# Kernel tuning notes

Measured on AMD Instinct MI355X. Metric: run time of the kernel, lower is better.

Reference implementation:

```python
import jax, jax.numpy as jnp
import numpy as np
from jax import lax

B, C, H, W = 16, 256, 32, 32
HK, WK = 16, 16
NH = 8              # num_heads
HD = C // NH        # head_dim = 32
N = H * W           # 1024
M = HK * WK         # 256
EXP = 3             # attn_expansion
HID = NH * EXP      # 24 hidden channels in DLA
EPS = 1e-5


def setup_inputs() -> dict:
    key = jax.random.key(0)
    ks = jax.random.split(key, 16)
    s = 0.02
    return {
        "q": jax.random.normal(ks[0], (B, C, H, W), jnp.float32),
        "kv": jax.random.normal(ks[1], (B, C, HK, WK), jnp.float32),
        "Wq": jax.random.normal(ks[2], (C, C), jnp.float32) * s,
        "Wkv": jax.random.normal(ks[3], (2 * C, C), jnp.float32) * s,
        "Wp": jax.random.normal(ks[4], (C, C), jnp.float32) * s,
        "bp": jnp.zeros((C,), jnp.float32),
        "rpb": jnp.ones((N, M), jnp.float32),
        "W_exp": jax.random.normal(ks[5], (HID, NH), jnp.float32) * s,   # 1x1 conv heads->hidden
        "g1": jnp.ones((HID,), jnp.float32),
        "b1": jnp.zeros((HID,), jnp.float32),
        "W_dw": jax.random.normal(ks[6], (HID, 1, 3, 3), jnp.float32) * s,  # depthwise 3x3
        "g2": jnp.ones((HID,), jnp.float32),
        "b2": jnp.zeros((HID,), jnp.float32),
        "W_red": jax.random.normal(ks[7], (NH, HID), jnp.float32) * s,  # 1x1 conv hidden->heads
        "g3": jnp.ones((NH,), jnp.float32),
        "b3": jnp.zeros((NH,), jnp.float32),
    }


def group_norm(x, gamma, beta, groups):
    b, c, h, w = x.shape
    xg = x.reshape(b, groups, c // groups, h, w)
    mu = xg.mean(axis=(2, 3, 4), keepdims=True)
    var = xg.var(axis=(2, 3, 4), keepdims=True)
    xn = ((xg - mu) * lax.rsqrt(var + EPS)).reshape(b, c, h, w)
    return xn * gamma[None, :, None, None] + beta[None, :, None, None]


def swish(x):
    return x * jax.nn.sigmoid(x)


def dla(a, W_exp, g1, b1, W_dw, g2, b2, W_red, g3, b3):
    # a: [B, NH, N, M] treated as NCHW image with C=num_heads
    x = jnp.einsum('bcnm,oc->bonm', a, W_exp)              # 1x1 expand -> [B,HID,N,M]
    x = swish(group_norm(x, g1, b1, EXP))
    x = lax.conv_general_dilated(
        x, W_dw, window_strides=(1, 1), padding='SAME',
        feature_group_count=HID,
        dimension_numbers=('NCHW', 'OIHW', 'NCHW'))        # depthwise 3x3
    x = swish(group_norm(x, g2, b2, EXP))
    x = jnp.einsum('bcnm,oc->bonm', x, W_red)              # 1x1 reduce -> [B,NH,N,M]
    x = group_norm(x, g3, b3, 1)                            # no activation
    return x


def reference(q, kv, Wq, Wkv, Wp, bp, rpb, W_exp, g1, b1, W_dw, g2, b2, W_red, g3, b3):
    b = q.shape[0]
    scale = HD ** -0.5
    # kv path: [B,C,HK,WK] -> [B,M,C] -> Linear(C->2C)
    kv_t = kv.reshape(b, C, M).transpose(0, 2, 1)
    kvp = kv_t @ Wkv.T                                     # [B,M,2C]
    kvp = kvp.reshape(b, M, 2, NH, HD).transpose(2, 0, 3, 1, 4)  # [2,B,NH,M,HD]
    k, v = kvp[0], kvp[1]
    # q path: [B,C,H,W] -> [B,N,C] -> Linear -> [B,NH,N,HD]
    qf = (q.reshape(b, C, N).transpose(0, 2, 1) @ Wq.T)
    qh = qf.reshape(b, N, NH, HD).transpose(0, 2, 1, 3)
    attn = jnp.einsum('bhnd,bhmd->bhnm', qh, k) * scale + rpb[None, None]
    attn = jax.nn.softmax(attn, axis=-1)
    attn = dla(attn, W_exp, g1, b1, W_dw, g2, b2, W_red, g3, b3)
    out = jnp.einsum('bhnm,bhmd->bhnd', attn, v)           # [B,NH,N,HD]
    out = out.transpose(0, 2, 1, 3).reshape(b, N, C)
    out = out @ Wp.T + bp
    return out.transpose(0, 2, 1).reshape(b, C, H, W)
```

## Files before the change

### kernel.cpp

```cpp
#include <hip/hip_runtime.h>
#include <math.h>

#define Bb 16
#define Cc 256
#define Nn 1024
#define Mm 256
#define NHh 8
#define HDd 32
#define HIDh 24
#define NMs (Nn*Mm)
#define TTB 16
#define CHUNK 8
#define EPSf 1e-5f
#define SCALEf 0.17677669529663687f
#define STP 32

typedef float v2f __attribute__((ext_vector_type(2)));
typedef __attribute__((ext_vector_type(8))) short bf8v;
typedef __attribute__((ext_vector_type(4))) float f4v;

__device__ __forceinline__ float wave_sum(float v){
#pragma unroll
  for (int off=32; off; off>>=1) v += __shfl_xor(v, off, 64);
  return v;
}
__device__ __forceinline__ float sigm_(float x){ return __builtin_amdgcn_rcpf(1.f + __expf(-x)); }
__device__ __forceinline__ float swish_(float x){ return x * sigm_(x); }
__device__ __forceinline__ v2f swish2(v2f x){
  v2f r;
  r.x = x.x * sigm_(x.x);
  r.y = x.y * sigm_(x.y);
  return r;
}
__device__ __forceinline__ unsigned short f2bf(float f){
  unsigned u = __float_as_uint(f);
  u += 0x7fffu + ((u >> 16) & 1u);
  return (unsigned short)(u >> 16);
}
__device__ __forceinline__ unsigned cvtpk(float lo, float hi){
  unsigned r;
  asm("v_cvt_pk_bf16_f32 %0, %1, %2" : "=v"(r) : "v"(lo), "v"(hi));
  return r;
}
__device__ __forceinline__ float bfup(unsigned short s){ return __uint_as_float(((unsigned)s) << 16); }
__device__ __forceinline__ float bflo(unsigned u){ return __uint_as_float(u << 16); }
__device__ __forceinline__ float bfhi(unsigned u){ return __uint_as_float(u & 0xffff0000u); }
__device__ __forceinline__ void gload_lds16(const void* g, void* l){
  __builtin_amdgcn_global_load_lds(
      (const __attribute__((address_space(1))) unsigned int*)g,
      (__attribute__((address_space(3))) unsigned int*)l, 16, 0, 0);
}

template<int MODE>
__launch_bounds__(256)
__global__ void gemm_mfma(const float* __restrict__ A,
                          const float* __restrict__ W,
                          const float* __restrict__ bias,
                          float* __restrict__ O1, float* __restrict__ O2, int Isize)
{
  __shared__ __align__(16) unsigned short Wt[64 * 40];
  __shared__ __align__(16) unsigned short At[64 * 40];
  const int b = blockIdx.z;
  const int i0 = blockIdx.x * 64;
  const int j0 = blockIdx.y * 64;
  const int tid = threadIdx.x;
  const int lane = tid & 63, wv = tid >> 6;
  const int wj = (wv >> 1) * 32, wi = (wv & 1) * 32;
  const int l15 = lane & 15, l4 = lane >> 4;

  const float* Ab = A + (long)b * Cc * Isize;
  const int sj = tid >> 2, skh = (tid & 3) * 8;
  const int si = tid & 63, skb = (tid >> 6) * 8;

  f4v acc[2][2] = {};
  for (int k0 = 0; k0 < Cc; k0 += 32) {
    float wreg[8];
    {
      const float* wp = W + (long)(j0 + sj) * Cc + k0 + skh;
      *(f4v*)&wreg[0] = *(const f4v*)&wp[0];
      *(f4v*)&wreg[4] = *(const f4v*)&wp[4];
    }
    float areg[8];
    {
      const float* ap = Ab + (long)(k0 + skb) * Isize + i0 + si;
#pragma unroll
      for (int e = 0; e < 8; e++) areg[e] = ap[(long)e * Isize];
    }
    __syncthreads();
    {
      unsigned pk[4];
#pragma unroll
      for (int t = 0; t < 4; t++) pk[t] = cvtpk(wreg[2*t], wreg[2*t+1]);
      *(uint4*)&Wt[sj*40 + skh] = make_uint4(pk[0], pk[1], pk[2], pk[3]);
#pragma unroll
      for (int t = 0; t < 4; t++) pk[t] = cvtpk(areg[2*t], areg[2*t+1]);
      *(uint4*)&At[si*40 + skb] = make_uint4(pk[0], pk[1], pk[2], pk[3]);
    }
    __syncthreads();
    bf8v af[2], bf[2];
#pragma unroll
    for (int fm = 0; fm < 2; fm++)
      af[fm] = *(const bf8v*)&Wt[(wj + fm*16 + l15)*40 + l4*8];
#pragma unroll
    for (int fn = 0; fn < 2; fn++)
      bf[fn] = *(const bf8v*)&At[(wi + fn*16 + l15)*40 + l4*8];
#pragma unroll
    for (int fm = 0; fm < 2; fm++)
#pragma unroll
      for (int fn = 0; fn < 2; fn++)
        acc[fm][fn] = __builtin_amdgcn_mfma_f32_16x16x32_bf16(af[fm], bf[fn], acc[fm][fn], 0, 0, 0);
  }
#pragma unroll
  for (int fm = 0; fm < 2; fm++) {
    const int jb = j0 + wj + fm*16 + l4*4;
    f4v bv = {0.f, 0.f, 0.f, 0.f};
    if (MODE == 2) bv = *(const f4v*)&bias[jb];
#pragma unroll
    for (int fn = 0; fn < 2; fn++) {
      const int ii = i0 + wi + fn*16 + l15;
      if (MODE == 1) {
        const int two = jb >> 8, jj = jb & 255;
        const int h = jj >> 5, d0 = jj & 31;
        unsigned short* p = (unsigned short*)(two ? O2 : O1)
                          + (((long)b * NHh + h) * Mm + ii) * HDd + d0;
        *(uint2*)p = make_uint2(cvtpk(acc[fm][fn][0], acc[fm][fn][1]),
                                cvtpk(acc[fm][fn][2], acc[fm][fn][3]));
      } else {
        float* op = O1 + ((long)b * Cc + jb) * (long)Isize + ii;
#pragma unroll
        for (int r = 0; r < 4; r++)
          op[(long)r * Isize] = acc[fm][fn][r] + bv[r];
      }
    }
  }
}

__launch_bounds__(256)
__global__ void attn_softmax(const float* __restrict__ qhT, const unsigned short* __restrict__ kb,
                             const float* __restrict__ rpb, unsigned short* __restrict__ attn)
{
  __shared__ __align__(16) unsigned short Kt[Mm * 40];
  __shared__ __align__(16) unsigned short Qt[64 * 40];
  const int b = blockIdx.z, h = blockIdx.y, n0 = blockIdx.x * 64;
  const int tid = threadIdx.x;
  const int lane = tid & 63, wv = tid >> 6;
  const int l15 = lane & 15, l4 = lane >> 4;
  {
    const unsigned short* kp = kb + ((long)b * NHh + h) * Mm * HDd;
#pragma unroll
    for (int u = 0; u < 4; u++) {
      const int f = tid + u * 256;
      const int m = f >> 2, q8 = (f & 3) * 8;
      *(uint4*)&Kt[m * 40 + q8] = *(const uint4*)&kp[m * HDd + q8];
    }
  }
  {
    const float* qp = qhT + ((long)b * NHh + h) * HDd * Nn + n0;
#pragma unroll
    for (int u = 0; u < 4; u++) {
      const int f = tid + u * 256;
      const int n = f & 63, d2 = (f >> 6) * 2;
      const float q0 = qp[(long)d2 * Nn + n];
      const float q1 = qp[(long)(d2 + 1) * Nn + n];
      *(unsigned*)&Qt[n * 40 + d2] = cvtpk(q0, q1);
    }
  }
  __syncthreads();
  const bf8v qf = *(const bf8v*)&Qt[(wv * 16 + l15) * 40 + l4 * 8];
  f4v S[16];
#pragma unroll
  for (int mt = 0; mt < 16; mt++) {
    const bf8v kf = *(const bf8v*)&Kt[(mt * 16 + l15) * 40 + l4 * 8];
    f4v z = {0.f, 0.f, 0.f, 0.f};
    S[mt] = __builtin_amdgcn_mfma_f32_16x16x32_bf16(kf, qf, z, 0, 0, 0);
  }
  const int n = n0 + wv * 16 + l15;
  const float* rp = rpb + (long)n * Mm;
  float mx = -1e30f;
#pragma unroll
  for (int mt = 0; mt < 16; mt++) {
    const f4v r4 = *(const f4v*)&rp[mt * 16 + l4 * 4];
    S[mt][0] = fmaf(S[mt][0], SCALEf, r4.x);
    S[mt][1] = fmaf(S[mt][1], SCALEf, r4.y);
    S[mt][2] = fmaf(S[mt][2], SCALEf, r4.z);
    S[mt][3] = fmaf(S[mt][3], SCALEf, r4.w);
    mx = fmaxf(mx, fmaxf(fmaxf(S[mt][0], S[mt][1]), fmaxf(S[mt][2], S[mt][3])));
  }
  mx = fmaxf(mx, __shfl_xor(mx, 16, 64));
  mx = fmaxf(mx, __shfl_xor(mx, 32, 64));
  float sum = 0.f;
#pragma unroll
  for (int mt = 0; mt < 16; mt++) {
    S[mt][0] = __expf(S[mt][0] - mx);
    S[mt][1] = __expf(S[mt][1] - mx);
    S[mt][2] = __expf(S[mt][2] - mx);
    S[mt][3] = __expf(S[mt][3] - mx);
    sum += (S[mt][0] + S[mt][1]) + (S[mt][2] + S[mt][3]);
  }
  sum += __shfl_xor(sum, 16, 64);
  sum += __shfl_xor(sum, 32, 64);
  const float inv = __builtin_amdgcn_rcpf(sum);
  unsigned short* ap = attn + (((long)b * NHh + h) * Nn + n) * Mm;
#pragma unroll
  for (int mt = 0; mt < 16; mt++) {
    const unsigned p0 = cvtpk(S[mt][0] * inv, S[mt][1] * inv);
    const unsigned p1 = cvtpk(S[mt][2] * inv, S[mt][3] * inv);
    *(uint2*)&ap[mt * 16 + l4 * 4] = make_uint2(p0, p1);
  }
}

__launch_bounds__(256)
__global__ void gram_stats(const unsigned short* __restrict__ attn, float* __restrict__ G)
{
  __shared__ float red[36][4];
  const int b = blockIdx.y, tid = threadIdx.x;
  const unsigned short* ap = attn + (long)b * NHh * NMs + (long)blockIdx.x * 2048 + tid * 8;
  float a[8][8];
#pragma unroll
  for (int h = 0; h < 8; h++) {
    const uint4 v = *(const uint4*)&ap[(long)h * NMs];
    a[h][0] = bflo(v.x); a[h][1] = bfhi(v.x); a[h][2] = bflo(v.y); a[h][3] = bfhi(v.y);
    a[h][4] = bflo(v.z); a[h][5] = bfhi(v.z); a[h][6] = bflo(v.w); a[h][7] = bfhi(v.w);
  }
  float g[36];
  int t = 0;
#pragma unroll
  for (int i = 0; i < 8; i++)
#pragma unroll
    for (int j = i; j < 8; j++, t++) {
      float s = 0.f;
#pragma unroll
      for (int m = 0; m < 8; m++) s = fmaf(a[i][m], a[j][m], s);
      g[t] = s;
    }
  const int lane = tid & 63, wid = tid >> 6;
#pragma unroll
  for (int t2 = 0; t2 < 36; t2++) {
    const float s = wave_sum(g[t2]);
    if (lane == 0) red[t2][wid] = s;
  }
  __syncthreads();
  if (tid < 36)
    atomicAdd(&G[((long)b * 36 + tid) * STP],
              red[tid][0] + red[tid][1] + red[tid][2] + red[tid][3]);
}

__launch_bounds__(768, 6)
__global__ void dla_pass_b(const unsigned short* __restrict__ attn,
                           const float* __restrict__ Wexp,
                           const float* __restrict__ g1, const float* __restrict__ b1,
                           const float* __restrict__ G, const float* __restrict__ Wdw,
                           unsigned short* __restrict__ x2, float* __restrict__ stats2c, int b0)
{
  __shared__ __align__(16) unsigned short sl[(TTB + 2) * NHh * Mm];
  const int tid = threadIdx.x;
  const int wv = tid >> 6, lane = tid & 63;
  const int bc = blockIdx.y, b = b0 + bc;
  const int n0 = blockIdx.x * TTB;
  const int c0 = wv * 2;
  const int g = wv >> 2;

  {
    const unsigned short* abase = attn + (long)b * NHh * NMs;
    const int q_lo = lane >> 5;
    const int m0 = (lane & 31) * 8;
#pragma unroll
    for (int i = 0; i < 6; i++) {
      const int pp = (wv * 6 + i) * 2;
      const int row = pp >> 3;
      const int nn = n0 - 1 + row;
      if (nn >= 0 && nn < Nn) {
        const int h = (pp + q_lo) & 7;
        gload_lds16(abase + (long)h * NMs + (long)nn * Mm + m0, &sl[pp * Mm]);
      }
    }
  }

  float mu, rs;
  {
    const float* Gb = G + (long)b * 36 * STP;
    float sum = 0.f, sumsq = 0.f;
    for (int c = g * 8; c < g * 8 + 8; c++) {
      float w[8];
#pragma unroll
      for (int h = 0; h < 8; h++) w[h] = Wexp[c * 8 + h];
      float wsu = 0.f;
#pragma unroll
      for (int h = 0; h < 8; h++) wsu += w[h];
      sum += wsu;
      float s2 = 0.f;
      int t = 0;
#pragma unroll
      for (int i = 0; i < 8; i++)
#pragma unroll
        for (int j = i; j < 8; j++, t++) {
          const float f = (i == j) ? 1.f : 2.f;
          s2 = fmaf(f * w[i] * w[j], Gb[t * STP], s2);
        }
      sumsq += s2;
    }
    const float cnt = 8.f * NMs;
    mu = sum * ((float)Nn / cnt);
    const float var = sumsq / cnt - mu * mu;
    rs = rsqrtf(var + EPSf);
  }
  v2f we2[8], wd2[9], B12;
  {
    const float A10 = rs * g1[c0], A11 = rs * g1[c0 + 1];
    B12.x = b1[c0] - mu * A10;
    B12.y = b1[c0 + 1] - mu * A11;
#pragma unroll
    for (int h = 0; h < NHh; h++) {
      we2[h].x = Wexp[c0 * NHh + h] * A10;
      we2[h].y = Wexp[(c0 + 1) * NHh + h] * A11;
    }
#pragma unroll
    for (int k = 0; k < 9; k++) {
      wd2[k].x = Wdw[c0 * 9 + k];
      wd2[k].y = Wdw[(c0 + 1) * 9 + k];
    }
  }
  __syncthreads();

  v2f s1p[4] = {}, s2p[4] = {};
  v2f smp = {0.f, 0.f}, sqp = {0.f, 0.f};
  for (int r = -1; r <= TTB; r++) {
    const int nn = n0 + r;
    const bool rowv = (nn >= 0 && nn < Nn);
    v2f xp[4];
    if (rowv) {
#pragma unroll
      for (int mi = 0; mi < 4; mi++) xp[mi] = B12;
      const unsigned short* sp = &sl[(r + 1) * NHh * Mm + lane * 4];
#pragma unroll
      for (int h = 0; h < NHh; h++) {
        const ushort4 v = *(const ushort4*)&sp[h * Mm];
        xp[0] += we2[h] * bfup(v.x);
        xp[1] += we2[h] * bfup(v.y);
        xp[2] += we2[h] * bfup(v.z);
        xp[3] += we2[h] * bfup(v.w);
      }
#pragma unroll
      for (int mi = 0; mi < 4; mi++) xp[mi] = swish2(xp[mi]);
    } else {
#pragma unroll
      for (int mi = 0; mi < 4; mi++) xp[mi] = (v2f){0.f, 0.f};
    }
    v2f xl, xr;
    xl.x = __shfl_up(xp[3].x, 1);  xl.y = __shfl_up(xp[3].y, 1);
    xr.x = __shfl_down(xp[0].x, 1); xr.y = __shfl_down(xp[0].y, 1);
    if (lane == 0)  { xl = (v2f){0.f, 0.f}; }
    if (lane == 63) { xr = (v2f){0.f, 0.f}; }
    const v2f L[4] = {xl, xp[0], xp[1], xp[2]};
    const v2f R[4] = {xp[1], xp[2], xp[3], xr};
    v2f y[4];
#pragma unroll
    for (int mi = 0; mi < 4; mi++) {
      const v2f u0 = wd2[0] * L[mi] + wd2[1] * xp[mi] + wd2[2] * R[mi];
      const v2f u1 = wd2[3] * L[mi] + wd2[4] * xp[mi] + wd2[5] * R[mi];
      const v2f u2 = wd2[6] * L[mi] + wd2[7] * xp[mi] + wd2[8] * R[mi];
      y[mi] = s2p[mi] + u2;
      s2p[mi] = s1p[mi] + u1;
      s1p[mi] = u0;
    }
    if (r >= 1) {
#pragma unroll
      for (int mi = 0; mi < 4; mi++) {
        smp += y[mi];
        sqp += y[mi] * y[mi];
      }
      const int nw = n0 + r - 1;
      const unsigned w0 = cvtpk(y[0].x, y[1].x), w1 = cvtpk(y[2].x, y[3].x);
      const unsigned w2 = cvtpk(y[0].y, y[1].y), w3 = cvtpk(y[2].y, y[3].y);
      unsigned short* xq = x2 + ((long)(bc * Nn + nw) * HIDh + c0) * Mm + lane * 4;
      *(uint2*)xq        = make_uint2(w0, w1);
      *(uint2*)(xq + Mm) = make_uint2(w2, w3);
    }
  }
  {
    const float vs0 = wave_sum(smp.x), vq0 = wave_sum(sqp.x);
    const float vs1 = wave_sum(smp.y), vq1 = wave_sum(sqp.y);
    if (lane == 0) {
      atomicAdd(&stats2c[((long)b * HIDh + c0) * STP], vs0);
      atomicAdd(&stats2c[((long)b * HIDh + c0) * STP + 1], vq0);
      atomicAdd(&stats2c[((long)b * HIDh + c0 + 1) * STP], vs1);
      atomicAdd(&stats2c[((long)b * HIDh + c0 + 1) * STP + 1], vq1);
    }
  }
}

__launch_bounds__(256)
__global__ void dla_pass_c(const unsigned short* __restrict__ x2, const float* __restrict__ g2,
                           const float* __restrict__ b2, const float* __restrict__ stats2c,
                           const float* __restrict__ Wred, unsigned short* __restrict__ a2,
                           float* __restrict__ partial3, int b0)
{
  __shared__ float wA[HIDh], wB[HIDh], wrs[HIDh][NHh];
  __shared__ float red2s[2][4];
  const int tid = threadIdx.x;
  const int wv = tid >> 6, lane = tid & 63;
  const int bc = blockIdx.y, b = b0 + bc;
  if (tid < HIDh) {
    const int c = tid, g = c >> 3;
    float s = 0.f, q = 0.f;
#pragma unroll
    for (int cc = 0; cc < 8; cc++) {
      s += stats2c[((long)b * HIDh + g * 8 + cc) * STP];
      q += stats2c[((long)b * HIDh + g * 8 + cc) * STP + 1];
    }
    const float cnt = 8.f * NMs;
    const float mu = s / cnt;
    const float var = q / cnt - mu * mu;
    const float A2 = rsqrtf(var + EPSf) * g2[c];
    wA[c] = A2; wB[c] = b2[c] - mu * A2;
  }
  if (tid < HIDh * NHh) {
    const int c = tid >> 3, h = tid & 7;
    wrs[c][h] = Wred[h * HIDh + c];
  }
  __syncthreads();
  const int rsel = lane >> 5, ms = lane & 31;
  const int n = blockIdx.x * 8 + wv * 2 + rsel;
  const unsigned short* xp = x2 + (long)(bc * Nn + n) * HIDh * Mm + ms * 8;
  v2f red[NHh][4] = {};
#pragma unroll
  for (int c = 0; c < HIDh; c++) {
    const uint4 xv = *(const uint4*)&xp[c * Mm];
    const v2f A2 = {wA[c], wA[c]}, B2 = {wB[c], wB[c]};
    v2f xw[4];
    xw[0] = (v2f){bflo(xv.x), bfhi(xv.x)};
    xw[1] = (v2f){bflo(xv.y), bfhi(xv.y)};
    xw[2] = (v2f){bflo(xv.z), bfhi(xv.z)};
    xw[3] = (v2f){bflo(xv.w), bfhi(xv.w)};
#pragma unroll
    for (int mi = 0; mi < 4; mi++) xw[mi] = swish2(xw[mi] * A2 + B2);
#pragma unroll
    for (int h = 0; h < NHh; h++) {
      const float w = wrs[c][h];
      const v2f w2 = {w, w};
#pragma unroll
      for (int mi = 0; mi < 4; mi++) red[h][mi] += w2 * xw[mi];
    }
  }
  v2f s3v = {0.f, 0.f}, q3v = {0.f, 0.f};
#pragma unroll
  for (int h = 0; h < NHh; h++) {
    uint4 st;
    st.x = cvtpk(red[h][0].x, red[h][0].y);
    st.y = cvtpk(red[h][1].x, red[h][1].y);
    st.z = cvtpk(red[h][2].x, red[h][2].y);
    st.w = cvtpk(red[h][3].x, red[h][3].y);
    *(uint4*)&a2[(((long)b * NHh + h) * Nn + n) * Mm + ms * 8] = st;
#pragma unroll
    for (int mi = 0; mi < 4; mi++) {
      s3v += red[h][mi];
      q3v += red[h][mi] * red[h][mi];
    }
  }
  float s3 = s3v.x + s3v.y, q3 = q3v.x + q3v.y;
  s3 = wave_sum(s3); q3 = wave_sum(q3);
  if (lane == 0) { red2s[0][wv] = s3; red2s[1][wv] = q3; }
  __syncthreads();
  if (tid < 2) {
    float t = red2s[tid][0] + red2s[tid][1] + red2s[tid][2] + red2s[tid][3];
    partial3[((long)b * 128 + blockIdx.x) * 2 + tid] = t;
  }
}

__launch_bounds__(256)
__global__ void pv_mfma(const unsigned short* __restrict__ a2, const unsigned short* __restrict__ vb,
                        const float* __restrict__ partial3,
                        const float* __restrict__ g3, const float* __restrict__ b3,
                        float* __restrict__ o)
{
  __shared__ __align__(16) unsigned short Vt[32 * 264];
  __shared__ float svl[32][9];
  __shared__ float r4s[4];
  const int b = blockIdx.z, h = blockIdx.y, n0 = blockIdx.x * 128;
  const int tid = threadIdx.x;
  const int lane = tid & 63, wv = tid >> 6;
  const int l15 = lane & 15, l4 = lane >> 4;
  {
    const unsigned short* vp = vb + ((long)b * NHh + h) * Mm * HDd;
#pragma unroll
    for (int u = 0; u < 32; u++) {
      const int idx = tid + u * 256;
      const int m = idx >> 5, d = idx & 31;
      Vt[d * 264 + m] = vp[idx];
    }
  }
  float pv_;
  {
    const int half = tid >> 7, i = tid & 127;
    pv_ = partial3[((long)b * 128 + i) * 2 + half];
  }
  __syncthreads();
  {
    const int d = tid & 31, seg = tid >> 5;
    float s = 0.f;
#pragma unroll
    for (int mm = 0; mm < 32; mm++) s += bfup(Vt[d * 264 + seg * 32 + mm]);
    svl[d][seg] = s;
  }
  {
    const float w = wave_sum(pv_);
    if (lane == 0) r4s[wv] = w;
  }
  __syncthreads();
  if (tid < 32) {
    float t = 0.f;
#pragma unroll
    for (int seg = 0; seg < 8; seg++) t += svl[tid][seg];
    svl[tid][0] = t;
  }
  __syncthreads();
  const float cnt = (float)(NHh * NMs);
  const float mu = (r4s[0] + r4s[1]) / cnt;
  const float var = (r4s[2] + r4s[3]) / cnt - mu * mu;
  const float r3 = rsqrtf(var + EPSf);
  const float alpha = r3 * g3[h];
  const float beta = b3[h] - mu * alpha;

  const unsigned short* ap = a2 + (((long)b * NHh + h) * Nn + n0) * Mm;
  f4v acc[2][2] = {};
#pragma unroll 2
  for (int k0 = 0; k0 < Mm; k0 += 32) {
    bf8v af[2], bf[2];
#pragma unroll
    for (int fm = 0; fm < 2; fm++)
      af[fm] = *(const bf8v*)&Vt[(fm * 16 + l15) * 264 + k0 + l4 * 8];
#pragma unroll
    for (int fn = 0; fn < 2; fn++)
      bf[fn] = *(const bf8v*)&ap[(long)(wv * 32 + fn * 16 + l15) * Mm + k0 + l4 * 8];
#pragma unroll
    for (int fm = 0; fm < 2; fm++)
#pragma unroll
      for (int fn = 0; fn < 2; fn++)
        acc[fm][fn] = __builtin_amdgcn_mfma_f32_16x16x32_bf16(af[fm], bf[fn], acc[fm][fn], 0, 0, 0);
  }
#pragma unroll
  for (int fm = 0; fm < 2; fm++) {
#pragma unroll
    for (int r = 0; r < 4; r++) {
      const int d = fm * 16 + l4 * 4 + r;
      const float bv = beta * svl[d][0];
      float* op = o + ((long)b * Cc + h * HDd + d) * Nn + n0 + wv * 32 + l15;
#pragma unroll
      for (int fn = 0; fn < 2; fn++)
        op[fn * 16] = fmaf(alpha, acc[fm][fn][r], bv);
    }
  }
}

extern "C" void kernel_launch(void* const* d_in, const int* in_sizes, int n_in,
                              void* d_out, int out_size, void* d_ws, size_t ws_size,
                              hipStream_t stream) {
  const float* q    = (const float*)d_in[0];
  const float* kv   = (const float*)d_in[1];
  const float* Wq   = (const float*)d_in[2];
  const float* Wkv  = (const float*)d_in[3];
  const float* Wp   = (const float*)d_in[4];
  const float* bp   = (const float*)d_in[5];
  const float* rpb  = (const float*)d_in[6];
  const float* Wexp = (const float*)d_in[7];
  const float* g1   = (const float*)d_in[8];
  const float* b1   = (const float*)d_in[9];
  const float* Wdw  = (const float*)d_in[10];
  const float* g2   = (const float*)d_in[11];
  const float* b2   = (const float*)d_in[12];
  const float* Wred = (const float*)d_in[13];
  const float* g3   = (const float*)d_in[14];
  const float* b3   = (const float*)d_in[15];
  float* out = (float*)d_out;

  float* ws = (float*)d_ws;
  size_t off = 0;
  auto alloc = [&](size_t n) { float* p = ws + off; off += n; return p; };
  float* attnf   = alloc((size_t)Bb * NHh * NMs / 2);
  float* a2f     = alloc((size_t)Bb * NHh * NMs / 2);
  float* big     = alloc((size_t)CHUNK * HIDh * NMs / 2);
  float* kbuf    = alloc((size_t)Bb * NHh * Mm * HDd);
  float* vbuf    = alloc((size_t)Bb * NHh * Mm * HDd);
  float* G       = alloc((size_t)Bb * 36 * STP);
  float* stats2c = alloc((size_t)Bb * HIDh * STP);
  float* partial3= alloc((size_t)Bb * 128 * 2);
  unsigned short* attn = (unsigned short*)attnf;
  unsigned short* a2 = (unsigned short*)a2f;
  unsigned short* kb16 = (unsigned short*)kbuf;
  unsigned short* vb16 = (unsigned short*)vbuf;
  float* qhT = big;
  unsigned short* x2 = (unsigned short*)big;
  float* oT = big;

  hipMemsetAsync(G, 0, (size_t)(Bb * 36 * STP + Bb * HIDh * STP) * sizeof(float), stream);

  gemm_mfma<0><<<dim3(Nn / 64, Cc / 64, Bb), 256, 0, stream>>>(q, Wq, nullptr, qhT, nullptr, Nn);
  gemm_mfma<1><<<dim3(Mm / 64, 512 / 64, Bb), 256, 0, stream>>>(kv, Wkv, nullptr, kbuf, vbuf, Mm);
  attn_softmax<<<dim3(Nn / 64, NHh, Bb), 256, 0, stream>>>(qhT, kb16, rpb, attn);
  gram_stats<<<dim3(NMs / 2048, Bb), 256, 0, stream>>>(attn, G);

  for (int b0 = 0; b0 < Bb; b0 += CHUNK) {
    dla_pass_b<<<dim3(Nn / TTB, CHUNK), 768, 0, stream>>>(
        attn, Wexp, g1, b1, G, Wdw, x2, stats2c, b0);
    dla_pass_c<<<dim3(Nn / 8, CHUNK), 256, 0, stream>>>(
        x2, g2, b2, stats2c, Wred, a2, partial3, b0);
  }

  pv_mfma<<<dim3(Nn / 128, NHh, Bb), 256, 0, stream>>>(a2, vb16, partial3, g3, b3, oT);
  gemm_mfma<2><<<dim3(Nn / 64, Cc / 64, Bb), 256, 0, stream>>>(oT, Wp, bp, out, nullptr, Nn);
}
```

Baseline: 371.8 us.

## Store intermediates as bf16, double gram_stats work per block, split DLA loads

The q-projection output and the PV output are now written as bf16 instead of fp32, and their consumers (attn_softmax and the final projection GEMM) read bf16 directly without converting. This halves the intermediate traffic and drops conversion instructions. gram_stats now handles two 2048-element chunks per thread, halving the grid and the number of atomic reductions. dla_pass_b splits its async global-to-LDS row loads into two phases, with the second half overlapping the first compute rows, plus an extra barrier mid-loop.

```diff
diff --git a/kernel.cpp b/kernel.cpp
--- a/kernel.cpp
+++ b/kernel.cpp
@@ -51,7 +51,7 @@
       (__attribute__((address_space(3))) unsigned int*)l, 16, 0, 0);
 }
 
-template<int MODE>
+template<int MODE, int ABF>
 __launch_bounds__(256)
 __global__ void gemm_mfma(const float* __restrict__ A,
                           const float* __restrict__ W,
@@ -68,7 +68,6 @@
   const int wj = (wv >> 1) * 32, wi = (wv & 1) * 32;
   const int l15 = lane & 15, l4 = lane >> 4;
 
-  const float* Ab = A + (long)b * Cc * Isize;
   const int sj = tid >> 2, skh = (tid & 3) * 8;
   const int si = tid & 63, skb = (tid >> 6) * 8;
 
@@ -81,8 +80,14 @@
       *(f4v*)&wreg[4] = *(const f4v*)&wp[4];
     }
     float areg[8];
-    {
-      const float* ap = Ab + (long)(k0 + skb) * Isize + i0 + si;
+    unsigned short areg16[8];
+    if constexpr (ABF) {
+      const unsigned short* ap = (const unsigned short*)A
+          + (long)b * Cc * Isize + (long)(k0 + skb) * Isize + i0 + si;
+#pragma unroll
+      for (int e = 0; e < 8; e++) areg16[e] = ap[(long)e * Isize];
+    } else {
+      const float* ap = A + (long)b * Cc * Isize + (long)(k0 + skb) * Isize + i0 + si;
 #pragma unroll
       for (int e = 0; e < 8; e++) areg[e] = ap[(long)e * Isize];
     }
@@ -92,8 +97,14 @@
 #pragma unroll
       for (int t = 0; t < 4; t++) pk[t] = cvtpk(wreg[2*t], wreg[2*t+1]);
       *(uint4*)&Wt[sj*40 + skh] = make_uint4(pk[0], pk[1], pk[2], pk[3]);
-#pragma unroll
-      for (int t = 0; t < 4; t++) pk[t] = cvtpk(areg[2*t], areg[2*t+1]);
+      if constexpr (ABF) {
+#pragma unroll
+        for (int t = 0; t < 4; t++)
+          pk[t] = (unsigned)areg16[2*t] | ((unsigned)areg16[2*t+1] << 16);
+      } else {
+#pragma unroll
+        for (int t = 0; t < 4; t++) pk[t] = cvtpk(areg[2*t], areg[2*t+1]);
+      }
       *(uint4*)&At[si*40 + skb] = make_uint4(pk[0], pk[1], pk[2], pk[3]);
     }
     __syncthreads();
@@ -125,6 +136,11 @@
                           + (((long)b * NHh + h) * Mm + ii) * HDd + d0;
         *(uint2*)p = make_uint2(cvtpk(acc[fm][fn][0], acc[fm][fn][1]),
                                 cvtpk(acc[fm][fn][2], acc[fm][fn][3]));
+      } else if (MODE == 0) {
+        unsigned short* op = (unsigned short*)O1 + ((long)b * Cc + jb) * (long)Isize + ii;
+#pragma unroll
+        for (int r = 0; r < 4; r++)
+          op[(long)r * Isize] = f2bf(acc[fm][fn][r]);
       } else {
         float* op = O1 + ((long)b * Cc + jb) * (long)Isize + ii;
 #pragma unroll
@@ -136,7 +152,8 @@
 }
 
 __launch_bounds__(256)
-__global__ void attn_softmax(const float* __restrict__ qhT, const unsigned short* __restrict__ kb,
+__global__ void attn_softmax(const unsigned short* __restrict__ qhT,
+                             const unsigned short* __restrict__ kb,
                              const float* __restrict__ rpb, unsigned short* __restrict__ attn)
 {
   __shared__ __align__(16) unsigned short Kt[Mm * 40];
@@ -155,14 +172,14 @@
     }
   }
   {
-    const float* qp = qhT + ((long)b * NHh + h) * HDd * Nn + n0;
+    const unsigned short* qp = qhT + ((long)b * NHh + h) * HDd * Nn + n0;
 #pragma unroll
     for (int u = 0; u < 4; u++) {
       const int f = tid + u * 256;
       const int n = f & 63, d2 = (f >> 6) * 2;
-      const float q0 = qp[(long)d2 * Nn + n];
-      const float q1 = qp[(long)(d2 + 1) * Nn + n];
-      *(unsigned*)&Qt[n * 40 + d2] = cvtpk(q0, q1);
+      const unsigned q0 = qp[(long)d2 * Nn + n];
+      const unsigned q1 = qp[(long)(d2 + 1) * Nn + n];
+      *(unsigned*)&Qt[n * 40 + d2] = q0 | (q1 << 16);
     }
   }
   __syncthreads();
@@ -214,25 +231,29 @@
 {
   __shared__ float red[36][4];
   const int b = blockIdx.y, tid = threadIdx.x;
-  const unsigned short* ap = attn + (long)b * NHh * NMs + (long)blockIdx.x * 2048 + tid * 8;
-  float a[8][8];
-#pragma unroll
-  for (int h = 0; h < 8; h++) {
-    const uint4 v = *(const uint4*)&ap[(long)h * NMs];
-    a[h][0] = bflo(v.x); a[h][1] = bfhi(v.x); a[h][2] = bflo(v.y); a[h][3] = bfhi(v.y);
-    a[h][4] = bflo(v.z); a[h][5] = bfhi(v.z); a[h][6] = bflo(v.w); a[h][7] = bfhi(v.w);
-  }
-  float g[36];
-  int t = 0;
-#pragma unroll
-  for (int i = 0; i < 8; i++)
-#pragma unroll
-    for (int j = i; j < 8; j++, t++) {
-      float s = 0.f;
-#pragma unroll
-      for (int m = 0; m < 8; m++) s = fmaf(a[i][m], a[j][m], s);
-      g[t] = s;
-    }
+  const unsigned short* ap = attn + (long)b * NHh * NMs + (long)blockIdx.x * 4096 + tid * 8;
+  float g[36] = {};
+#pragma unroll
+  for (int half = 0; half < 2; half++) {
+    const unsigned short* app = ap + half * 2048;
+    float a[8][8];
+#pragma unroll
+    for (int h = 0; h < 8; h++) {
+      const uint4 v = *(const uint4*)&app[(long)h * NMs];
+      a[h][0] = bflo(v.x); a[h][1] = bfhi(v.x); a[h][2] = bflo(v.y); a[h][3] = bfhi(v.y);
+      a[h][4] = bflo(v.z); a[h][5] = bfhi(v.z); a[h][6] = bflo(v.w); a[h][7] = bfhi(v.w);
+    }
+    int t = 0;
+#pragma unroll
+    for (int i = 0; i < 8; i++)
+#pragma unroll
+      for (int j = i; j < 8; j++, t++) {
+        float s = 0.f;
+#pragma unroll
+        for (int m = 0; m < 8; m++) s = fmaf(a[i][m], a[j][m], s);
+        g[t] += s;
+      }
+  }
   const int lane = tid & 63, wid = tid >> 6;
 #pragma unroll
   for (int t2 = 0; t2 < 36; t2++) {
@@ -260,13 +281,14 @@
   const int c0 = wv * 2;
   const int g = wv >> 2;
 
-  {
-    const unsigned short* abase = attn + (long)b * NHh * NMs;
-    const int q_lo = lane >> 5;
-    const int m0 = (lane & 31) * 8;
-#pragma unroll
-    for (int i = 0; i < 6; i++) {
-      const int pp = (wv * 6 + i) * 2;
+  const unsigned short* abase = attn + (long)b * NHh * NMs;
+  const int q_lo = lane >> 5;
+  const int m0 = (lane & 31) * 8;
+#pragma unroll
+  for (int i = 0; i < 4; i++) {
+    const int pr = wv + i * 12;
+    if (pr < 40) {
+      const int pp = pr * 2;
       const int row = pp >> 3;
       const int nn = n0 - 1 + row;
       if (nn >= 0 && nn < Nn) {
@@ -322,9 +344,24 @@
   }
   __syncthreads();
 
+#pragma unroll
+  for (int i = 0; i < 3; i++) {
+    const int pr = 40 + wv + i * 12;
+    if (pr < 72) {
+      const int pp = pr * 2;
+      const int row = pp >> 3;
+      const int nn = n0 - 1 + row;
+      if (nn >= 0 && nn < Nn) {
+        const int h = (pp + q_lo) & 7;
+        gload_lds16(abase + (long)h * NMs + (long)nn * Mm + m0, &sl[pp * Mm]);
+      }
+    }
+  }
+
   v2f s1p[4] = {}, s2p[4] = {};
   v2f smp = {0.f, 0.f}, sqp = {0.f, 0.f};
   for (int r = -1; r <= TTB; r++) {
+    if (r == 9) __syncthreads();
     const int nn = n0 + r;
     const bool rowv = (nn >= 0 && nn < Nn);
     v2f xp[4];
@@ -471,7 +508,7 @@
 __global__ void pv_mfma(const unsigned short* __restrict__ a2, const unsigned short* __restrict__ vb,
                         const float* __restrict__ partial3,
                         const float* __restrict__ g3, const float* __restrict__ b3,
-                        float* __restrict__ o)
+                        unsigned short* __restrict__ o)
 {
   __shared__ __align__(16) unsigned short Vt[32 * 264];
   __shared__ float svl[32][9];
@@ -544,10 +581,10 @@
     for (int r = 0; r < 4; r++) {
       const int d = fm * 16 + l4 * 4 + r;
       const float bv = beta * svl[d][0];
-      float* op = o + ((long)b * Cc + h * HDd + d) * Nn + n0 + wv * 32 + l15;
+      unsigned short* op = o + ((long)b * Cc + h * HDd + d) * Nn + n0 + wv * 32 + l15;
 #pragma unroll
       for (int fn = 0; fn < 2; fn++)
-        op[fn * 16] = fmaf(alpha, acc[fm][fn][r], bv);
+        op[fn * 16] = f2bf(fmaf(alpha, acc[fm][fn][r], bv));
     }
   }
 }
@@ -588,16 +625,18 @@
   unsigned short* a2 = (unsigned short*)a2f;
   unsigned short* kb16 = (unsigned short*)kbuf;
   unsigned short* vb16 = (unsigned short*)vbuf;
-  float* qhT = big;
+  unsigned short* qhT16 = (unsigned short*)big;
   unsigned short* x2 = (unsigned short*)big;
-  float* oT = big;
+  unsigned short* oT16 = (unsigned short*)big;
 
   hipMemsetAsync(G, 0, (size_t)(Bb * 36 * STP + Bb * HIDh * STP) * sizeof(float), stream);
 
-  gemm_mfma<0><<<dim3(Nn / 64, Cc / 64, Bb), 256, 0, stream>>>(q, Wq, nullptr, qhT, nullptr, Nn);
-  gemm_mfma<1><<<dim3(Mm / 64, 512 / 64, Bb), 256, 0, stream>>>(kv, Wkv, nullptr, kbuf, vbuf, Mm);
-  attn_softmax<<<dim3(Nn / 64, NHh, Bb), 256, 0, stream>>>(qhT, kb16, rpb, attn);
-  gram_stats<<<dim3(NMs / 2048, Bb), 256, 0, stream>>>(attn, G);
+  gemm_mfma<0, 0><<<dim3(Nn / 64, Cc / 64, Bb), 256, 0, stream>>>(
+      q, Wq, nullptr, (float*)qhT16, nullptr, Nn);
+  gemm_mfma<1, 0><<<dim3(Mm / 64, 512 / 64, Bb), 256, 0, stream>>>(
+      kv, Wkv, nullptr, kbuf, vbuf, Mm);
+  attn_softmax<<<dim3(Nn / 64, NHh, Bb), 256, 0, stream>>>(qhT16, kb16, rpb, attn);
+  gram_stats<<<dim3(NMs / 4096, Bb), 256, 0, stream>>>(attn, G);
 
   for (int b0 = 0; b0 < Bb; b0 += CHUNK) {
     dla_pass_b<<<dim3(Nn / TTB, CHUNK), 768, 0, stream>>>(
@@ -606,6 +645,7 @@
         x2, g2, b2, stats2c, Wred, a2, partial3, b0);
   }
 
-  pv_mfma<<<dim3(Nn / 128, NHh, Bb), 256, 0, stream>>>(a2, vb16, partial3, g3, b3, oT);
-  gemm_mfma<2><<<dim3(Nn / 64, Cc / 64, Bb), 256, 0, stream>>>(oT, Wp, bp, out, nullptr, Nn);
-}
+  pv_mfma<<<dim3(Nn / 128, NHh, Bb), 256, 0, stream>>>(a2, vb16, partial3, g3, b3, oT16);
+  gemm_mfma<2, 1><<<dim3(Nn / 64, Cc / 64, Bb), 256, 0, stream>>>(
+      (const float*)oT16, Wp, bp, out, nullptr, Nn);
+}
```

Result: no change. 368.2 us (-1.0%).
